# Optimization experiments

Measured on AMD Instinct MI355X. Metric: run time of the kernel, lower is better.

Reference implementation:

```python
import jax, jax.numpy as jnp
import numpy as np


def setup_inputs() -> dict:
    B, S, DK, DV, H = 2, 2048, 1024, 1024, 16
    ks = jax.random.split(jax.random.key(0), 7)
    keys = jax.random.normal(ks[0], (B, S, DK), jnp.float32)
    queries = jax.random.normal(ks[1], (B, S, DK), jnp.float32)
    values = jax.random.normal(ks[2], (B, S, DV), jnp.float32)
    # per-head projection weights, stored as [H, in, out] (torch Linear uses W.T; math-equivalent)
    WQ = jax.random.normal(ks[3], (H, DK, DK // H), jnp.float32) / np.sqrt(DK).astype(np.float32)
    WK = jax.random.normal(ks[4], (H, DK, DK // H), jnp.float32) / np.sqrt(DK).astype(np.float32)
    WV = jax.random.normal(ks[5], (H, DV, DV // H), jnp.float32) / np.sqrt(DV).astype(np.float32)
    WO = jax.random.normal(ks[6], (DV, DV), jnp.float32) / np.sqrt(DV).astype(np.float32)
    return {"keys": keys, "queries": queries, "values": values,
            "WQ": WQ, "WK": WK, "WV": WV, "WO": WO, "masking": 1}


def reference(keys, queries, values, WQ, WK, WV, WO, masking):
    B, Sq, _ = queries.shape
    Sk = keys.shape[1]
    # batched per-head projections (original loops over heads in Python)
    Q = jnp.einsum('bqd,hde->bhqe', queries, WQ)   # [B,H,Sq,dh]
    K = jnp.einsum('bkd,hde->bhke', keys, WK)      # [B,H,Sk,dh]
    V = jnp.einsum('bkd,hde->bhke', values, WV)    # [B,H,Sk,dvh]
    q_idx = jnp.arange(Sq)[:, None]
    k_idx = jnp.arange(Sk)[None, :]
    causal = k_idx <= q_idx
    # NOTE: original never applies the slope m; bias = (i - j) for i<=j else 0, same for all heads
    bias = jnp.where(causal, (k_idx - q_idx).astype(jnp.float32), 0.0)
    scale = np.float32(1.0 / np.sqrt(Sk))  # original divides by sqrt(keys.shape[1])
    y = (jnp.einsum('bhqe,bhke->bhqk', Q, K) + bias) * scale
    if masking:
        y = jnp.where(causal, y, -jnp.inf)
    # original: F.softmax(y, 1) on [B,Sq,Sk] -> softmax over the QUERY axis
    z = jax.nn.softmax(y, axis=2)
    out = jnp.einsum('bhqk,bhke->bhqe', z, V)      # [B,H,Sq,dvh]
    out = out.transpose(0, 2, 1, 3).reshape(B, Sq, -1)  # concat heads on last dim
    return out @ WO
```

## Files before the change

### kernel.cpp

```cpp
#include <hip/hip_runtime.h>
#include <math.h>

#define SEQ    2048
#define DMODEL 1024
#define NH     16
#define DH     64
#define NB     2
#define BHN    (NB*NH)

static constexpr float SCALE = 0.02209708691207961f;

typedef __attribute__((ext_vector_type(8))) short short8;
typedef __attribute__((ext_vector_type(4))) short short4v;
typedef __attribute__((ext_vector_type(4))) float f32x4;

__device__ __forceinline__ short f2bf(float f) {
    union { float f; unsigned u; } v; v.f = f;
    unsigned r = (v.u + 0x7FFFu + ((v.u >> 16) & 1u)) >> 16;
    return (short)r;
}

__device__ __forceinline__ unsigned pack_bf2(float a, float b) {
    union { float f; unsigned u; } ua, ub; ua.f = a; ub.f = b;
    return __builtin_amdgcn_perm(ub.u + 0x8000u, ua.u + 0x8000u, 0x07060302u);
}

__device__ __forceinline__ float bf2f(short s) {
    union { unsigned u; float f; } v; v.u = ((unsigned)(unsigned short)s) << 16;
    return v.f;
}

__device__ __forceinline__ void load16_lds(const short* g, short* l) {
    __builtin_amdgcn_global_load_lds(
        (const __attribute__((address_space(1))) unsigned int*)g,
        (__attribute__((address_space(3))) unsigned int*)l,
        16, 0, 0);
}

__device__ __forceinline__ void stage_rows(const short* g, short* s, int t, int ldg, int nIter) {
    int wave = t >> 6, lane = t & 63;
    #pragma unroll
    for (int i = 0; i < 4; ++i) {
        if (i >= nIter) break;
        int E   = i * 2048 + wave * 512 + lane * 8;
        int row = E >> 6;
        int blk = (lane & 7) ^ (row & 7);
        load16_lds(g + (size_t)row * ldg + blk * 8, s + i * 2048 + wave * 512);
    }
}

__device__ __forceinline__ short8 frag_sw(const short* s, int rowbase, int ks, int lane) {
    int m   = rowbase + (lane & 15);
    int q   = lane >> 4;
    int blk = (ks * 4 + q) ^ (m & 7);
    return *(const short8*)(s + m * 64 + blk * 8);
}

__device__ __forceinline__ void swizzle_tile(int x, int y, int& tile, int& bh) {
    int r = y >> 3;
    bh = (y & 7) * 4 + r;
    int xs = (r & 2) ? ((x + 16) & 31) : x;
    tile = (r & 1) ? (31 - xs) : xs;
}

__global__ __launch_bounds__(256) void convert_x(
    const float* __restrict__ q, const float* __restrict__ k, const float* __restrict__ v,
    short* __restrict__ Xq, short* __restrict__ Xk, short* __restrict__ Xv)
{
    const int z = blockIdx.z;
    const float* src = (z == 0) ? q : (z == 1) ? k : v;
    short* dst = (z == 0) ? Xq : (z == 1) ? Xk : Xv;
    size_t idx = ((size_t)blockIdx.x * 256 + threadIdx.x) * 8;
    float4 a = *(const float4*)(src + idx);
    float4 b = *(const float4*)(src + idx + 4);
    short8 o;
    o[0] = f2bf(a.x); o[1] = f2bf(a.y); o[2] = f2bf(a.z); o[3] = f2bf(a.w);
    o[4] = f2bf(b.x); o[5] = f2bf(b.y); o[6] = f2bf(b.z); o[7] = f2bf(b.w);
    *(short8*)(dst + idx) = o;
}

__global__ __launch_bounds__(256) void convert_w(
    const float* __restrict__ WQ, const float* __restrict__ WK,
    const float* __restrict__ WV, const float* __restrict__ WO,
    short* __restrict__ WQt, short* __restrict__ WKt,
    short* __restrict__ WVt, short* __restrict__ WOt)
{
    const int z = blockIdx.z;
    const int k0 = blockIdx.x * 64;
    const int ny = blockIdx.y;
    const float* W = (z == 0) ? WQ : (z == 1) ? WK : (z == 2) ? WV : WO;
    short* Wt = (z == 0) ? WQt : (z == 1) ? WKt : (z == 2) ? WVt : WOt;

    __shared__ float Ts[64][68];
    const int t = threadIdx.x;
    const int tr = t >> 4, tc4 = (t & 15) * 4;

    #pragma unroll
    for (int i = 0; i < 4; ++i) {
        int row = tr + i * 16;
        float4 v;
        if (z < 3) v = *(const float4*)(W + (size_t)ny * DMODEL * DH + (size_t)(k0 + row) * DH + tc4);
        else       v = *(const float4*)(W + (size_t)(k0 + row) * DMODEL + ny * 64 + tc4);
        Ts[tc4 + 0][row] = v.x; Ts[tc4 + 1][row] = v.y;
        Ts[tc4 + 2][row] = v.z; Ts[tc4 + 3][row] = v.w;
    }
    __syncthreads();
    #pragma unroll
    for (int i = 0; i < 4; ++i) {
        int nl = tr + i * 16;
        short4v o;
        o[0] = f2bf(Ts[nl][tc4 + 0]); o[1] = f2bf(Ts[nl][tc4 + 1]);
        o[2] = f2bf(Ts[nl][tc4 + 2]); o[3] = f2bf(Ts[nl][tc4 + 3]);
        *(short4v*)(Wt + (size_t)(ny * 64 + nl) * DMODEL + k0 + tc4) = o;
    }
}

__global__ __launch_bounds__(256) void gemm_nt(
    const short* __restrict__ A0, const short* __restrict__ A1, const short* __restrict__ A2,
    const short* __restrict__ B0, const short* __restrict__ B1, const short* __restrict__ B2,
    short* __restrict__ Y0, short* __restrict__ Y1, short* __restrict__ Y2,
    float* __restrict__ outF, int phase)
{
    const int z = blockIdx.z;
    const short* X  = (phase == 1) ? A0 : (z == 0) ? A0 : (z == 1) ? A1 : A2;
    const short* Wt = (phase == 1) ? B0 : (z == 0) ? B0 : (z == 1) ? B1 : B2;
    short* Y        = (z == 0) ? Y0 : (z == 1) ? Y1 : Y2;
    const bool vOrient = (phase == 0) && (z == 2);

    const int n0 = blockIdx.x * 128;
    const int m0 = blockIdx.y * 128;

    __shared__ short As[128 * 64];
    __shared__ short Bs[128 * 64];

    const int t = threadIdx.x;
    const int wave = t >> 6, lane = t & 63;
    const int wrow = (wave >> 1) * 64, wcol = (wave & 1) * 64;
    const int quad = lane >> 4, l15 = lane & 15;

    f32x4 acc[4][4];
    #pragma unroll
    for (int i = 0; i < 4; ++i)
        #pragma unroll
        for (int j = 0; j < 4; ++j)
            acc[i][j] = (f32x4)0.f;

    for (int k0 = 0; k0 < DMODEL; k0 += 64) {
        __syncthreads();
        stage_rows(X  + (size_t)m0 * DMODEL + k0, As, t, DMODEL, 4);
        stage_rows(Wt + (size_t)n0 * DMODEL + k0, Bs, t, DMODEL, 4);
        __syncthreads();
        if (!vOrient) {
            #pragma unroll
            for (int ks = 0; ks < 2; ++ks) {
                short8 xf[4], wf[4];
                #pragma unroll
                for (int i = 0; i < 4; ++i) xf[i] = frag_sw(As, wrow + i * 16, ks, lane);
                #pragma unroll
                for (int i = 0; i < 4; ++i) wf[i] = frag_sw(Bs, wcol + i * 16, ks, lane);
                #pragma unroll
                for (int a = 0; a < 4; ++a)
                    #pragma unroll
                    for (int b = 0; b < 4; ++b)
                        acc[a][b] = __builtin_amdgcn_mfma_f32_16x16x32_bf16(
                            wf[a], xf[b], acc[a][b], 0, 0, 0);
            }
        } else {
            #pragma unroll
            for (int ks = 0; ks < 2; ++ks) {
                short8 xf[4], wf[4];
                #pragma unroll
                for (int i = 0; i < 4; ++i) xf[i] = frag_sw(As, wrow + i * 16, ks, lane);
                #pragma unroll
                for (int i = 0; i < 4; ++i) wf[i] = frag_sw(Bs, wcol + i * 16, ks, lane);
                #pragma unroll
                for (int a = 0; a < 4; ++a)
                    #pragma unroll
                    for (int b = 0; b < 4; ++b)
                        acc[a][b] = __builtin_amdgcn_mfma_f32_16x16x32_bf16(
                            xf[a], wf[b], acc[a][b], 0, 0, 0);
            }
        }
    }

    if (vOrient) {
        #pragma unroll
        for (int a = 0; a < 4; ++a) {
            #pragma unroll
            for (int b = 0; b < 4; ++b) {
                int m = m0 + wrow + a * 16 + quad * 4;
                int n = n0 + wcol + b * 16 + l15;
                int bb = m >> 11, s = m & 2047, h = n >> 6, e = n & 63;
                short4v o;
                #pragma unroll
                for (int i = 0; i < 4; ++i) o[i] = f2bf(acc[a][b][i]);
                *(short4v*)(Y + ((size_t)((bb * NH + h) * DH + e)) * SEQ + s) = o;
            }
        }
    } else if (phase == 1) {
        #pragma unroll
        for (int a = 0; a < 4; ++a) {
            #pragma unroll
            for (int b = 0; b < 4; ++b) {
                int n = n0 + wcol + a * 16 + quad * 4;
                int m = m0 + wrow + b * 16 + l15;
                float4 o = make_float4(acc[a][b][0], acc[a][b][1], acc[a][b][2], acc[a][b][3]);
                *(float4*)(outF + (size_t)m * DMODEL + n) = o;
            }
        }
    } else {
        #pragma unroll
        for (int a = 0; a < 4; ++a) {
            #pragma unroll
            for (int b = 0; b < 4; ++b) {
                int n = n0 + wcol + a * 16 + quad * 4;
                int m = m0 + wrow + b * 16 + l15;
                int bb = m >> 11, s = m & 2047, h = n >> 6, e = n & 63;
                short4v o;
                #pragma unroll
                for (int i = 0; i < 4; ++i) o[i] = f2bf(acc[a][b][i]);
                *(short4v*)(Y + ((size_t)((bb * NH + h) * SEQ + s)) * DH + e) = o;
            }
        }
    }
}

__global__ __launch_bounds__(256) void stats_mfma(
    const short* __restrict__ Qg, const short* __restrict__ Kg,
    float* __restrict__ rDg, const int* __restrict__ mask_p)
{
    int kt, bh;
    swizzle_tile(blockIdx.x, blockIdx.y, kt, bh);
    const int k0 = kt * 64;
    const int masking = mask_p[0];

    __shared__ short Ks[64 * 64];
    __shared__ short Qs[2][128 * 64];

    const int t = threadIdx.x;
    const int wave = t >> 6, lane = t & 63;
    const int quad = lane >> 4, l15 = lane & 15;

    const int qb0 = masking ? (kt >> 1) : 0;
    const int q0s = qb0 * 128;
    stage_rows(Kg + ((size_t)bh * SEQ + k0) * DH, Ks, t, DH, 2);
    stage_rows(Qg + ((size_t)bh * SEQ + q0s) * DH, Qs[0], t, DH, 4);
    __syncthreads();

    short8 Kf[2];
    Kf[0] = frag_sw(Ks, wave * 16, 0, lane);
    Kf[1] = frag_sw(Ks, wave * 16, 1, lane);

    int   kgi[4];
    float biasK[4];
    #pragma unroll
    for (int i = 0; i < 4; ++i) {
        kgi[i] = k0 + wave * 16 + quad * 4 + i;
        biasK[i] = SCALE * (float)kgi[i];
    }
    float qS[8];
    #pragma unroll
    for (int nt = 0; nt < 8; ++nt)
        qS[nt] = SCALE * (float)(q0s + nt * 16 + l15);

    float dsum[4] = {0.f, 0.f, 0.f, 0.f};
    const int nIter = masking ? (16 - qb0) : 16;
    for (int it = 0; it < nIter; ++it) {
        const int cur = it & 1;
        if (it > 0) __syncthreads();
        if (it + 1 < nIter)
            stage_rows(Qg + ((size_t)bh * SEQ + q0s + (it + 1) * 128) * DH, Qs[1 - cur], t, DH, 4);

        f32x4 acc[8];
        #pragma unroll
        for (int nt = 0; nt < 8; ++nt) acc[nt] = (f32x4)0.f;
        __builtin_amdgcn_s_setprio(1);
        #pragma unroll
        for (int ks = 0; ks < 2; ++ks)
            #pragma unroll
            for (int nt = 0; nt < 8; ++nt)
                acc[nt] = __builtin_amdgcn_mfma_f32_16x16x32_bf16(
                    Kf[ks], frag_sw(Qs[cur], nt * 16, ks, lane), acc[nt], 0, 0, 0);
        __builtin_amdgcn_s_setprio(0);

        const bool exact = masking && (it == 0);
        #pragma unroll
        for (int nt = 0; nt < 8; ++nt) {
            #pragma unroll
            for (int i = 0; i < 4; ++i) {
                float diff = biasK[i] - qS[nt];
                float v = masking ? fmaf(acc[nt][i], SCALE, diff)
                                  : fmaf(acc[nt][i], SCALE, fminf(diff, 0.f));
                float e = __expf(v);
                if (exact)
                    e = (kgi[i] <= (q0s + nt * 16 + l15)) ? e : 0.f;
                dsum[i] += e;
            }
        }
        #pragma unroll
        for (int nt = 0; nt < 8; ++nt) qS[nt] += 128.f * SCALE;
    }

    #pragma unroll
    for (int i = 0; i < 4; ++i) {
        float d = dsum[i];
        #pragma unroll
        for (int mm = 1; mm < 16; mm <<= 1) d += __shfl_xor(d, mm);
        dsum[i] = d;
    }
    if (l15 == 0) {
        const int kc = k0 + wave * 16 + quad * 4;
        float4 o = make_float4(1.f / dsum[0], 1.f / dsum[1], 1.f / dsum[2], 1.f / dsum[3]);
        *(float4*)(rDg + (size_t)bh * SEQ + kc) = o;
    }
}

__global__ __launch_bounds__(256) void scale_vt(
    short* __restrict__ Vt, const float* __restrict__ rDg)
{
    size_t base = ((size_t)blockIdx.x * 256 + threadIdx.x) * 8;
    int s = (int)(base & (SEQ - 1));
    int bh = (int)(base >> 17);
    short8 v = *(short8*)(Vt + base);
    const float* rp = rDg + (size_t)bh * SEQ + s;
    float4 r0 = *(const float4*)rp;
    float4 r1 = *(const float4*)(rp + 4);
    float rr[8] = {r0.x, r0.y, r0.z, r0.w, r1.x, r1.y, r1.z, r1.w};
    union { unsigned u[4]; short8 s8; } o;
    #pragma unroll
    for (int j = 0; j < 4; ++j)
        o.u[j] = pack_bf2(bf2f(v[2 * j]) * rr[2 * j], bf2f(v[2 * j + 1]) * rr[2 * j + 1]);
    *(short8*)(Vt + base) = o.s8;
}

template<int MODE>
__device__ __forceinline__ void attn_tile(
    const short* Kbuf, const short* Vbuf, short* Pw,
    const short8 Qf[2], const float bias[4][4], f32x4 oacc[4],
    int lane, int quad, int l15, int qloc)
{
    f32x4 sacc[4];
    #pragma unroll
    for (int mt = 0; mt < 4; ++mt) sacc[mt] = (f32x4)0.f;
    #pragma unroll
    for (int ks = 0; ks < 2; ++ks) {
        #pragma unroll
        for (int mt = 0; mt < 4; ++mt)
            sacc[mt] = __builtin_amdgcn_mfma_f32_16x16x32_bf16(
                frag_sw(Kbuf, mt * 16, ks, lane), Qf[ks], sacc[mt], 0, 0, 0);
    }
    __asm__ volatile("" ::: "memory");
    #pragma unroll
    for (int mt = 0; mt < 4; ++mt) {
        float p[4];
        #pragma unroll
        for (int i = 0; i < 4; ++i) {
            float bi = bias[mt][i];
            float v = (MODE == 2) ? fmaf(sacc[mt][i], SCALE, fminf(bi, 0.f))
                                  : fmaf(sacc[mt][i], SCALE, bi);
            float e = __expf(v);
            if (MODE == 1)
                e = ((mt * 16 + quad * 4 + i) <= qloc) ? e : 0.f;
            p[i] = e;
        }
        int blk = (2 * mt + (quad >> 1)) ^ (l15 & 7);
        *(uint2*)(Pw + l15 * 64 + blk * 8 + (quad & 1) * 4) =
            make_uint2(pack_bf2(p[0], p[1]), pack_bf2(p[2], p[3]));
    }
    __asm__ volatile("" ::: "memory");
    #pragma unroll
    for (int ks = 0; ks < 2; ++ks) {
        short8 pf = *(const short8*)(Pw + l15 * 64 + (((ks * 4 + quad) ^ (l15 & 7)) * 8));
        #pragma unroll
        for (int mt = 0; mt < 4; ++mt)
            oacc[mt] = __builtin_amdgcn_mfma_f32_16x16x32_bf16(
                frag_sw(Vbuf, mt * 16, ks, lane), pf, oacc[mt], 0, 0, 0);
    }
}

__global__ __launch_bounds__(256) void attn_mfma(
    const short* __restrict__ Qg, const short* __restrict__ Kg, const short* __restrict__ Vt,
    short* __restrict__ attnb, const int* __restrict__ mask_p)
{
    int qt, bh;
    swizzle_tile(blockIdx.x, blockIdx.y, qt, bh);
    const int b = bh / NH, h = bh % NH;
    const int q0 = qt * 64;
    const int masking = mask_p[0];

    __shared__ short Qs[64 * 64];
    __shared__ short Ks[2][64 * 64];
    __shared__ short Vts[2][64 * 64];

    const int t = threadIdx.x;
    const int wave = t >> 6, lane = t & 63;
    const int quad = lane >> 4, l15 = lane & 15;
    short* Pw = Qs + wave * 1024;
    const int qloc = wave * 16 + l15;

    stage_rows(Qg + ((size_t)bh * SEQ + q0) * DH, Qs, t, DH, 2);
    stage_rows(Kg + (size_t)bh * SEQ * DH, Ks[0], t, DH, 2);
    stage_rows(Vt + (size_t)bh * DH * SEQ, Vts[0], t, SEQ, 2);
    __syncthreads();

    short8 Qf[2];
    Qf[0] = frag_sw(Qs, wave * 16, 0, lane);
    Qf[1] = frag_sw(Qs, wave * 16, 1, lane);

    float bias[4][4];
    #pragma unroll
    for (int mt = 0; mt < 4; ++mt)
        #pragma unroll
        for (int i = 0; i < 4; ++i)
            bias[mt][i] = SCALE * (float)((mt * 16 + quad * 4 + i)
                                        - (q0 + qloc));

    f32x4 oacc[4];
    #pragma unroll
    for (int mt = 0; mt < 4; ++mt) oacc[mt] = (f32x4)0.f;

    const int nIter = masking ? (qt + 1) : (SEQ / 64);
    for (int it = 0; it < nIter; ++it) {
        const int cur = it & 1;
        if (it > 0) __syncthreads();
        if (it + 1 < nIter) {
            const int k0n = (it + 1) * 64;
            stage_rows(Kg + ((size_t)bh * SEQ + k0n) * DH, Ks[1 - cur], t, DH, 2);
            stage_rows(Vt + (size_t)bh * DH * SEQ + k0n, Vts[1 - cur], t, SEQ, 2);
        }
        if (!masking)       attn_tile<2>(Ks[cur], Vts[cur], Pw, Qf, bias, oacc, lane, quad, l15, qloc);
        else if (it == qt)  attn_tile<1>(Ks[cur], Vts[cur], Pw, Qf, bias, oacc, lane, quad, l15, qloc);
        else                attn_tile<0>(Ks[cur], Vts[cur], Pw, Qf, bias, oacc, lane, quad, l15, qloc);
        #pragma unroll
        for (int mt = 0; mt < 4; ++mt)
            #pragma unroll
            for (int i = 0; i < 4; ++i)
                bias[mt][i] += 64.f * SCALE;
    }

    #pragma unroll
    for (int mt = 0; mt < 4; ++mt) {
        int e = mt * 16 + quad * 4;
        int q = q0 + wave * 16 + l15;
        short4v o;
        #pragma unroll
        for (int i = 0; i < 4; ++i) o[i] = f2bf(oacc[mt][i]);
        *(short4v*)(attnb + ((size_t)(b * SEQ + q)) * DMODEL + h * DH + e) = o;
    }
}

extern "C" void kernel_launch(void* const* d_in, const int* in_sizes, int n_in,
                              void* d_out, int out_size, void* d_ws, size_t ws_size,
                              hipStream_t stream) {
    const float* keys    = (const float*)d_in[0];
    const float* queries = (const float*)d_in[1];
    const float* values  = (const float*)d_in[2];
    const float* WQ      = (const float*)d_in[3];
    const float* WK      = (const float*)d_in[4];
    const float* WV      = (const float*)d_in[5];
    const float* WO      = (const float*)d_in[6];
    const int*   mask_p  = (const int*)d_in[7];
    float* out = (float*)d_out;

    const size_t nX = (size_t)NB * SEQ * DMODEL;
    const size_t nW = (size_t)DMODEL * DMODEL;
    const size_t nQ = (size_t)BHN * SEQ * DH;

    short* ws = (short*)d_ws;
    short* Xq    = ws;
    short* Xk    = Xq + nX;
    short* Xv    = Xk + nX;
    short* WQt   = Xv + nX;
    short* WKt   = WQt + nW;
    short* WVt   = WKt + nW;
    short* WOt   = WVt + nW;
    short* Qg    = WOt + nW;
    short* Kg    = Qg + nQ;
    short* Vtg   = Kg + nQ;
    short* attnb = Vtg + nQ;
    float* rDg   = (float*)(attnb + nX);

    convert_x<<<dim3(2048, 1, 3), dim3(256), 0, stream>>>(queries, keys, values, Xq, Xk, Xv);
    convert_w<<<dim3(16, 16, 4), dim3(256), 0, stream>>>(WQ, WK, WV, WO, WQt, WKt, WVt, WOt);
    gemm_nt<<<dim3(8, 32, 3), dim3(256), 0, stream>>>(
        Xq, Xk, Xv, WQt, WKt, WVt, Qg, Kg, Vtg, nullptr, 0);
    stats_mfma<<<dim3(32, 32), dim3(256), 0, stream>>>(Qg, Kg, rDg, mask_p);
    scale_vt<<<dim3(2048), dim3(256), 0, stream>>>(Vtg, rDg);
    attn_mfma<<<dim3(32, 32), dim3(256), 0, stream>>>(Qg, Kg, Vtg, attnb, mask_p);
    gemm_nt<<<dim3(8, 32, 1), dim3(256), 0, stream>>>(
        attnb, nullptr, nullptr, WOt, nullptr, nullptr, nullptr, nullptr, nullptr, out, 1);
}
```

Baseline: 270.1 us.

## Double query tile per attention block to reuse K/V fragments across two row groups

The attention kernel now processes 128 query rows per block, with each wave handling two 16-row groups, so every K and V fragment read from LDS feeds two MFMAs. This halves the number of blocks and the K/V staging traffic per query row. It also wraps the MFMA phases in s_setprio hints and adds per-wave causal tile skipping. In exchange it raises register pressure, halves the grid to 512 blocks (fewer waves resident to hide latency), and leaves idle waves on diagonal tiles where some waves skip their work.

```diff
diff --git a/kernel.cpp b/kernel.cpp
--- a/kernel.cpp
+++ b/kernel.cpp
@@ -61,6 +61,13 @@
     bh = (y & 7) * 4 + r;
     int xs = (r & 2) ? ((x + 16) & 31) : x;
     tile = (r & 1) ? (31 - xs) : xs;
+}
+
+__device__ __forceinline__ void swizzle_tile16(int x, int y, int& tile, int& bh) {
+    int r = y >> 3;
+    bh = (y & 7) * 4 + r;
+    int xs = (r & 1) ? ((x + 8) & 15) : x;
+    tile = (r & 2) ? (15 - xs) : xs;
 }
 
 __global__ __launch_bounds__(256) void convert_x(
@@ -334,48 +341,71 @@
 }
 
 template<int MODE>
-__device__ __forceinline__ void attn_tile(
+__device__ __forceinline__ void attn_tile2(
     const short* Kbuf, const short* Vbuf, short* Pw,
-    const short8 Qf[2], const float bias[4][4], f32x4 oacc[4],
-    int lane, int quad, int l15, int qloc)
-{
-    f32x4 sacc[4];
-    #pragma unroll
-    for (int mt = 0; mt < 4; ++mt) sacc[mt] = (f32x4)0.f;
+    const short8 Qf[2][2], const float biasK[4][4], const float qS[2],
+    const int qgi[2], int kbase, f32x4 oacc[4][2],
+    int lane, int quad, int l15)
+{
+    f32x4 sacc[4][2];
+    #pragma unroll
+    for (int mt = 0; mt < 4; ++mt)
+        #pragma unroll
+        for (int g = 0; g < 2; ++g) sacc[mt][g] = (f32x4)0.f;
+    __builtin_amdgcn_s_setprio(1);
     #pragma unroll
     for (int ks = 0; ks < 2; ++ks) {
         #pragma unroll
-        for (int mt = 0; mt < 4; ++mt)
-            sacc[mt] = __builtin_amdgcn_mfma_f32_16x16x32_bf16(
-                frag_sw(Kbuf, mt * 16, ks, lane), Qf[ks], sacc[mt], 0, 0, 0);
-    }
+        for (int mt = 0; mt < 4; ++mt) {
+            short8 kf = frag_sw(Kbuf, mt * 16, ks, lane);
+            #pragma unroll
+            for (int g = 0; g < 2; ++g)
+                sacc[mt][g] = __builtin_amdgcn_mfma_f32_16x16x32_bf16(
+                    kf, Qf[g][ks], sacc[mt][g], 0, 0, 0);
+        }
+    }
+    __builtin_amdgcn_s_setprio(0);
     __asm__ volatile("" ::: "memory");
     #pragma unroll
     for (int mt = 0; mt < 4; ++mt) {
-        float p[4];
-        #pragma unroll
-        for (int i = 0; i < 4; ++i) {
-            float bi = bias[mt][i];
-            float v = (MODE == 2) ? fmaf(sacc[mt][i], SCALE, fminf(bi, 0.f))
-                                  : fmaf(sacc[mt][i], SCALE, bi);
-            float e = __expf(v);
-            if (MODE == 1)
-                e = ((mt * 16 + quad * 4 + i) <= qloc) ? e : 0.f;
-            p[i] = e;
-        }
-        int blk = (2 * mt + (quad >> 1)) ^ (l15 & 7);
-        *(uint2*)(Pw + l15 * 64 + blk * 8 + (quad & 1) * 4) =
-            make_uint2(pack_bf2(p[0], p[1]), pack_bf2(p[2], p[3]));
+        #pragma unroll
+        for (int g = 0; g < 2; ++g) {
+            float p[4];
+            #pragma unroll
+            for (int i = 0; i < 4; ++i) {
+                float diff = biasK[mt][i] - qS[g];
+                float v = (MODE == 2) ? fmaf(sacc[mt][g][i], SCALE, fminf(diff, 0.f))
+                                      : fmaf(sacc[mt][g][i], SCALE, diff);
+                float e = __expf(v);
+                if (MODE == 1)
+                    e = ((kbase + mt * 16 + quad * 4 + i) <= qgi[g]) ? e : 0.f;
+                p[i] = e;
+            }
+            int row = g * 16 + l15;
+            int blk = (2 * mt + (quad >> 1)) ^ (l15 & 7);
+            *(uint2*)(Pw + row * 64 + blk * 8 + (quad & 1) * 4) =
+                make_uint2(pack_bf2(p[0], p[1]), pack_bf2(p[2], p[3]));
+        }
     }
     __asm__ volatile("" ::: "memory");
+    __builtin_amdgcn_s_setprio(1);
     #pragma unroll
     for (int ks = 0; ks < 2; ++ks) {
-        short8 pf = *(const short8*)(Pw + l15 * 64 + (((ks * 4 + quad) ^ (l15 & 7)) * 8));
-        #pragma unroll
-        for (int mt = 0; mt < 4; ++mt)
-            oacc[mt] = __builtin_amdgcn_mfma_f32_16x16x32_bf16(
-                frag_sw(Vbuf, mt * 16, ks, lane), pf, oacc[mt], 0, 0, 0);
-    }
+        short8 pf[2];
+        #pragma unroll
+        for (int g = 0; g < 2; ++g)
+            pf[g] = *(const short8*)(Pw + (g * 16 + l15) * 64
+                                     + (((ks * 4 + quad) ^ (l15 & 7)) * 8));
+        #pragma unroll
+        for (int mt = 0; mt < 4; ++mt) {
+            short8 vf = frag_sw(Vbuf, mt * 16, ks, lane);
+            #pragma unroll
+            for (int g = 0; g < 2; ++g)
+                oacc[mt][g] = __builtin_amdgcn_mfma_f32_16x16x32_bf16(
+                    vf, pf[g], oacc[mt][g], 0, 0, 0);
+        }
+    }
+    __builtin_amdgcn_s_setprio(0);
 }
 
 __global__ __launch_bounds__(256) void attn_mfma(
@@ -383,43 +413,53 @@
     short* __restrict__ attnb, const int* __restrict__ mask_p)
 {
     int qt, bh;
-    swizzle_tile(blockIdx.x, blockIdx.y, qt, bh);
+    swizzle_tile16(blockIdx.x, blockIdx.y, qt, bh);
     const int b = bh / NH, h = bh % NH;
-    const int q0 = qt * 64;
+    const int q0 = qt * 128;
     const int masking = mask_p[0];
 
-    __shared__ short Qs[64 * 64];
+    __shared__ short Qs[128 * 64];
     __shared__ short Ks[2][64 * 64];
     __shared__ short Vts[2][64 * 64];
 
     const int t = threadIdx.x;
     const int wave = t >> 6, lane = t & 63;
     const int quad = lane >> 4, l15 = lane & 15;
-    short* Pw = Qs + wave * 1024;
-    const int qloc = wave * 16 + l15;
-
-    stage_rows(Qg + ((size_t)bh * SEQ + q0) * DH, Qs, t, DH, 2);
+    short* Pw = Qs + wave * 2048;
+
+    stage_rows(Qg + ((size_t)bh * SEQ + q0) * DH, Qs, t, DH, 4);
     stage_rows(Kg + (size_t)bh * SEQ * DH, Ks[0], t, DH, 2);
     stage_rows(Vt + (size_t)bh * DH * SEQ, Vts[0], t, SEQ, 2);
     __syncthreads();
 
-    short8 Qf[2];
-    Qf[0] = frag_sw(Qs, wave * 16, 0, lane);
-    Qf[1] = frag_sw(Qs, wave * 16, 1, lane);
-
-    float bias[4][4];
+    short8 Qf[2][2];
+    #pragma unroll
+    for (int g = 0; g < 2; ++g) {
+        Qf[g][0] = frag_sw(Qs, wave * 32 + g * 16, 0, lane);
+        Qf[g][1] = frag_sw(Qs, wave * 32 + g * 16, 1, lane);
+    }
+
+    int   qgi[2];
+    float qS[2];
+    #pragma unroll
+    for (int g = 0; g < 2; ++g) {
+        qgi[g] = q0 + wave * 32 + g * 16 + l15;
+        qS[g]  = SCALE * (float)qgi[g];
+    }
+    float biasK[4][4];
     #pragma unroll
     for (int mt = 0; mt < 4; ++mt)
         #pragma unroll
         for (int i = 0; i < 4; ++i)
-            bias[mt][i] = SCALE * (float)((mt * 16 + quad * 4 + i)
-                                        - (q0 + qloc));
-
-    f32x4 oacc[4];
-    #pragma unroll
-    for (int mt = 0; mt < 4; ++mt) oacc[mt] = (f32x4)0.f;
-
-    const int nIter = masking ? (qt + 1) : (SEQ / 64);
+            biasK[mt][i] = SCALE * (float)(mt * 16 + quad * 4 + i);
+
+    f32x4 oacc[4][2];
+    #pragma unroll
+    for (int mt = 0; mt < 4; ++mt)
+        #pragma unroll
+        for (int g = 0; g < 2; ++g) oacc[mt][g] = (f32x4)0.f;
+
+    const int nIter = masking ? (2 * qt + 2) : (SEQ / 64);
     for (int it = 0; it < nIter; ++it) {
         const int cur = it & 1;
         if (it > 0) __syncthreads();
@@ -428,24 +468,34 @@
             stage_rows(Kg + ((size_t)bh * SEQ + k0n) * DH, Ks[1 - cur], t, DH, 2);
             stage_rows(Vt + (size_t)bh * DH * SEQ + k0n, Vts[1 - cur], t, SEQ, 2);
         }
-        if (!masking)       attn_tile<2>(Ks[cur], Vts[cur], Pw, Qf, bias, oacc, lane, quad, l15, qloc);
-        else if (it == qt)  attn_tile<1>(Ks[cur], Vts[cur], Pw, Qf, bias, oacc, lane, quad, l15, qloc);
-        else                attn_tile<0>(Ks[cur], Vts[cur], Pw, Qf, bias, oacc, lane, quad, l15, qloc);
+        if (!masking) {
+            attn_tile2<2>(Ks[cur], Vts[cur], Pw, Qf, biasK, qS, qgi, 64 * it,
+                          oacc, lane, quad, l15);
+        } else if (64 * it + 63 <= q0 + 32 * wave) {
+            attn_tile2<0>(Ks[cur], Vts[cur], Pw, Qf, biasK, qS, qgi, 64 * it,
+                          oacc, lane, quad, l15);
+        } else if (64 * it <= q0 + 32 * wave + 31) {
+            attn_tile2<1>(Ks[cur], Vts[cur], Pw, Qf, biasK, qS, qgi, 64 * it,
+                          oacc, lane, quad, l15);
+        }
         #pragma unroll
         for (int mt = 0; mt < 4; ++mt)
             #pragma unroll
             for (int i = 0; i < 4; ++i)
-                bias[mt][i] += 64.f * SCALE;
+                biasK[mt][i] += 64.f * SCALE;
     }
 
     #pragma unroll
     for (int mt = 0; mt < 4; ++mt) {
-        int e = mt * 16 + quad * 4;
-        int q = q0 + wave * 16 + l15;
-        short4v o;
-        #pragma unroll
-        for (int i = 0; i < 4; ++i) o[i] = f2bf(oacc[mt][i]);
-        *(short4v*)(attnb + ((size_t)(b * SEQ + q)) * DMODEL + h * DH + e) = o;
+        #pragma unroll
+        for (int g = 0; g < 2; ++g) {
+            int e = mt * 16 + quad * 4;
+            int q = q0 + wave * 32 + g * 16 + l15;
+            short4v o;
+            #pragma unroll
+            for (int i = 0; i < 4; ++i) o[i] = f2bf(oacc[mt][g][i]);
+            *(short4v*)(attnb + ((size_t)(b * SEQ + q)) * DMODEL + h * DH + e) = o;
+        }
     }
 }
 
@@ -486,7 +536,7 @@
         Xq, Xk, Xv, WQt, WKt, WVt, Qg, Kg, Vtg, nullptr, 0);
     stats_mfma<<<dim3(32, 32), dim3(256), 0, stream>>>(Qg, Kg, rDg, mask_p);
     scale_vt<<<dim3(2048), dim3(256), 0, stream>>>(Vtg, rDg);
-    attn_mfma<<<dim3(32, 32), dim3(256), 0, stream>>>(Qg, Kg, Vtg, attnb, mask_p);
+    attn_mfma<<<dim3(16, 32), dim3(256), 0, stream>>>(Qg, Kg, Vtg, attnb, mask_p);
     gemm_nt<<<dim3(8, 32, 1), dim3(256), 0, stream>>>(
         attnb, nullptr, nullptr, WOt, nullptr, nullptr, nullptr, nullptr, nullptr, out, 1);
 }
```

Result: no change. 269.7 us (-0.2%).

## Load attention K/V fragments directly from global memory, drop LDS staging

Applied to the files above, without the earlier changes.

The attention kernel no longer stages Q, K and V^T tiles into double-buffered shared memory with barriers. Each wave now loads its MFMA fragments straight from global memory (relying on L1/L2 for reuse across the four waves), and only the per-wave P scratch stays in LDS. It also raises wave priority around the MFMA blocks with s_setprio. This removes __syncthreads and LDS traffic and raises occupancy, at the cost of redundant global/L2 loads per wave, less coalesced strided V^T accesses, and no software prefetch to hide latency.

```diff
diff --git a/kernel.cpp b/kernel.cpp
--- a/kernel.cpp
+++ b/kernel.cpp
@@ -54,6 +54,12 @@
     int q   = lane >> 4;
     int blk = (ks * 4 + q) ^ (m & 7);
     return *(const short8*)(s + m * 64 + blk * 8);
+}
+
+__device__ __forceinline__ short8 frag_g(const short* base, int stride, int rowbase, int ks, int lane) {
+    int m = rowbase + (lane & 15);
+    int c = (lane >> 4) * 8 + ks * 32;
+    return *(const short8*)(base + (size_t)m * stride + c);
 }
 
 __device__ __forceinline__ void swizzle_tile(int x, int y, int& tile, int& bh) {
@@ -334,21 +340,23 @@
 }
 
 template<int MODE>
-__device__ __forceinline__ void attn_tile(
-    const short* Kbuf, const short* Vbuf, short* Pw,
+__device__ __forceinline__ void attn_tile_g(
+    const short* Kp, const short* Vp, short* Pw,
     const short8 Qf[2], const float bias[4][4], f32x4 oacc[4],
     int lane, int quad, int l15, int qloc)
 {
     f32x4 sacc[4];
     #pragma unroll
     for (int mt = 0; mt < 4; ++mt) sacc[mt] = (f32x4)0.f;
+    __builtin_amdgcn_s_setprio(1);
     #pragma unroll
     for (int ks = 0; ks < 2; ++ks) {
         #pragma unroll
         for (int mt = 0; mt < 4; ++mt)
             sacc[mt] = __builtin_amdgcn_mfma_f32_16x16x32_bf16(
-                frag_sw(Kbuf, mt * 16, ks, lane), Qf[ks], sacc[mt], 0, 0, 0);
-    }
+                frag_g(Kp, DH, mt * 16, ks, lane), Qf[ks], sacc[mt], 0, 0, 0);
+    }
+    __builtin_amdgcn_s_setprio(0);
     __asm__ volatile("" ::: "memory");
     #pragma unroll
     for (int mt = 0; mt < 4; ++mt) {
@@ -368,14 +376,16 @@
             make_uint2(pack_bf2(p[0], p[1]), pack_bf2(p[2], p[3]));
     }
     __asm__ volatile("" ::: "memory");
+    __builtin_amdgcn_s_setprio(1);
     #pragma unroll
     for (int ks = 0; ks < 2; ++ks) {
         short8 pf = *(const short8*)(Pw + l15 * 64 + (((ks * 4 + quad) ^ (l15 & 7)) * 8));
         #pragma unroll
         for (int mt = 0; mt < 4; ++mt)
             oacc[mt] = __builtin_amdgcn_mfma_f32_16x16x32_bf16(
-                frag_sw(Vbuf, mt * 16, ks, lane), pf, oacc[mt], 0, 0, 0);
-    }
+                frag_g(Vp, SEQ, mt * 16, ks, lane), pf, oacc[mt], 0, 0, 0);
+    }
+    __builtin_amdgcn_s_setprio(0);
 }
 
 __global__ __launch_bounds__(256) void attn_mfma(
@@ -388,24 +398,18 @@
     const int q0 = qt * 64;
     const int masking = mask_p[0];
 
-    __shared__ short Qs[64 * 64];
-    __shared__ short Ks[2][64 * 64];
-    __shared__ short Vts[2][64 * 64];
+    __shared__ short Ps[4 * 1024];
 
     const int t = threadIdx.x;
     const int wave = t >> 6, lane = t & 63;
     const int quad = lane >> 4, l15 = lane & 15;
-    short* Pw = Qs + wave * 1024;
+    short* Pw = Ps + wave * 1024;
     const int qloc = wave * 16 + l15;
 
-    stage_rows(Qg + ((size_t)bh * SEQ + q0) * DH, Qs, t, DH, 2);
-    stage_rows(Kg + (size_t)bh * SEQ * DH, Ks[0], t, DH, 2);
-    stage_rows(Vt + (size_t)bh * DH * SEQ, Vts[0], t, SEQ, 2);
-    __syncthreads();
-
+    const short* Qp = Qg + ((size_t)bh * SEQ + q0 + wave * 16) * DH;
     short8 Qf[2];
-    Qf[0] = frag_sw(Qs, wave * 16, 0, lane);
-    Qf[1] = frag_sw(Qs, wave * 16, 1, lane);
+    Qf[0] = frag_g(Qp, DH, 0, 0, lane);
+    Qf[1] = frag_g(Qp, DH, 0, 1, lane);
 
     float bias[4][4];
     #pragma unroll
@@ -419,18 +423,16 @@
     #pragma unroll
     for (int mt = 0; mt < 4; ++mt) oacc[mt] = (f32x4)0.f;
 
+    const short* Kp = Kg + (size_t)bh * SEQ * DH;
+    const short* Vp = Vt + (size_t)bh * DH * SEQ;
+
     const int nIter = masking ? (qt + 1) : (SEQ / 64);
     for (int it = 0; it < nIter; ++it) {
-        const int cur = it & 1;
-        if (it > 0) __syncthreads();
-        if (it + 1 < nIter) {
-            const int k0n = (it + 1) * 64;
-            stage_rows(Kg + ((size_t)bh * SEQ + k0n) * DH, Ks[1 - cur], t, DH, 2);
-            stage_rows(Vt + (size_t)bh * DH * SEQ + k0n, Vts[1 - cur], t, SEQ, 2);
-        }
-        if (!masking)       attn_tile<2>(Ks[cur], Vts[cur], Pw, Qf, bias, oacc, lane, quad, l15, qloc);
-        else if (it == qt)  attn_tile<1>(Ks[cur], Vts[cur], Pw, Qf, bias, oacc, lane, quad, l15, qloc);
-        else                attn_tile<0>(Ks[cur], Vts[cur], Pw, Qf, bias, oacc, lane, quad, l15, qloc);
+        const short* Kt = Kp + (size_t)it * 64 * DH;
+        const short* Vc = Vp + it * 64;
+        if (!masking)       attn_tile_g<2>(Kt, Vc, Pw, Qf, bias, oacc, lane, quad, l15, qloc);
+        else if (it == qt)  attn_tile_g<1>(Kt, Vc, Pw, Qf, bias, oacc, lane, quad, l15, qloc);
+        else                attn_tile_g<0>(Kt, Vc, Pw, Qf, bias, oacc, lane, quad, l15, qloc);
         #pragma unroll
         for (int mt = 0; mt < 4; ++mt)
             #pragma unroll
```

Result: slower. 347.3 us (+28.6%).

## Pair heavy and light causal tiles per block in stats and attention kernels

Applied to the files above, without the earlier changes.

Both stats_mfma and attn_mfma now launch 512 blocks. Each block processes two work items, w and 1023-w, so under the causal mask every block gets a roughly equal amount of work, replacing the earlier swizzled 32x32 grid. The attention tile also raises wave priority around its MFMA sections. This is meant to remove tail imbalance from triangular work. In exchange it halves the number of blocks, which may reduce occupancy and latency hiding on a GPU with 256 CUs.

```diff
diff --git a/kernel.cpp b/kernel.cpp
--- a/kernel.cpp
+++ b/kernel.cpp
@@ -54,13 +54,6 @@
     int q   = lane >> 4;
     int blk = (ks * 4 + q) ^ (m & 7);
     return *(const short8*)(s + m * 64 + blk * 8);
-}
-
-__device__ __forceinline__ void swizzle_tile(int x, int y, int& tile, int& bh) {
-    int r = y >> 3;
-    bh = (y & 7) * 4 + r;
-    int xs = (r & 2) ? ((x + 16) & 31) : x;
-    tile = (r & 1) ? (31 - xs) : xs;
 }
 
 __global__ __launch_bounds__(256) void convert_x(
@@ -229,9 +222,7 @@
     const short* __restrict__ Qg, const short* __restrict__ Kg,
     float* __restrict__ rDg, const int* __restrict__ mask_p)
 {
-    int kt, bh;
-    swizzle_tile(blockIdx.x, blockIdx.y, kt, bh);
-    const int k0 = kt * 64;
+    const int gblk = blockIdx.x;
     const int masking = mask_p[0];
 
     __shared__ short Ks[64 * 64];
@@ -241,77 +232,84 @@
     const int wave = t >> 6, lane = t & 63;
     const int quad = lane >> 4, l15 = lane & 15;
 
-    const int qb0 = masking ? (kt >> 1) : 0;
-    const int q0s = qb0 * 128;
-    stage_rows(Kg + ((size_t)bh * SEQ + k0) * DH, Ks, t, DH, 2);
-    stage_rows(Qg + ((size_t)bh * SEQ + q0s) * DH, Qs[0], t, DH, 4);
-    __syncthreads();
-
-    short8 Kf[2];
-    Kf[0] = frag_sw(Ks, wave * 16, 0, lane);
-    Kf[1] = frag_sw(Ks, wave * 16, 1, lane);
-
-    int   kgi[4];
-    float biasK[4];
-    #pragma unroll
-    for (int i = 0; i < 4; ++i) {
-        kgi[i] = k0 + wave * 16 + quad * 4 + i;
-        biasK[i] = SCALE * (float)kgi[i];
-    }
-    float qS[8];
-    #pragma unroll
-    for (int nt = 0; nt < 8; ++nt)
-        qS[nt] = SCALE * (float)(q0s + nt * 16 + l15);
-
-    float dsum[4] = {0.f, 0.f, 0.f, 0.f};
-    const int nIter = masking ? (16 - qb0) : 16;
-    for (int it = 0; it < nIter; ++it) {
-        const int cur = it & 1;
-        if (it > 0) __syncthreads();
-        if (it + 1 < nIter)
-            stage_rows(Qg + ((size_t)bh * SEQ + q0s + (it + 1) * 128) * DH, Qs[1 - cur], t, DH, 4);
-
-        f32x4 acc[8];
-        #pragma unroll
-        for (int nt = 0; nt < 8; ++nt) acc[nt] = (f32x4)0.f;
-        __builtin_amdgcn_s_setprio(1);
-        #pragma unroll
-        for (int ks = 0; ks < 2; ++ks)
-            #pragma unroll
-            for (int nt = 0; nt < 8; ++nt)
-                acc[nt] = __builtin_amdgcn_mfma_f32_16x16x32_bf16(
-                    Kf[ks], frag_sw(Qs[cur], nt * 16, ks, lane), acc[nt], 0, 0, 0);
-        __builtin_amdgcn_s_setprio(0);
-
-        const bool exact = masking && (it == 0);
-        #pragma unroll
-        for (int nt = 0; nt < 8; ++nt) {
-            #pragma unroll
-            for (int i = 0; i < 4; ++i) {
-                float diff = biasK[i] - qS[nt];
-                float v = masking ? fmaf(acc[nt][i], SCALE, diff)
-                                  : fmaf(acc[nt][i], SCALE, fminf(diff, 0.f));
-                float e = __expf(v);
-                if (exact)
-                    e = (kgi[i] <= (q0s + nt * 16 + l15)) ? e : 0.f;
-                dsum[i] += e;
-            }
-        }
-        #pragma unroll
-        for (int nt = 0; nt < 8; ++nt) qS[nt] += 128.f * SCALE;
-    }
-
-    #pragma unroll
-    for (int i = 0; i < 4; ++i) {
-        float d = dsum[i];
-        #pragma unroll
-        for (int mm = 1; mm < 16; mm <<= 1) d += __shfl_xor(d, mm);
-        dsum[i] = d;
-    }
-    if (l15 == 0) {
-        const int kc = k0 + wave * 16 + quad * 4;
-        float4 o = make_float4(1.f / dsum[0], 1.f / dsum[1], 1.f / dsum[2], 1.f / dsum[3]);
-        *(float4*)(rDg + (size_t)bh * SEQ + kc) = o;
+    for (int item = 0; item < 2; ++item) {
+        const int w  = item ? (1023 - gblk) : gblk;
+        const int kt = w >> 5, bh = w & 31;
+        const int k0 = kt * 64;
+
+        const int qb0 = masking ? (kt >> 1) : 0;
+        const int q0s = qb0 * 128;
+        if (item) __syncthreads();
+        stage_rows(Kg + ((size_t)bh * SEQ + k0) * DH, Ks, t, DH, 2);
+        stage_rows(Qg + ((size_t)bh * SEQ + q0s) * DH, Qs[0], t, DH, 4);
+        __syncthreads();
+
+        short8 Kf[2];
+        Kf[0] = frag_sw(Ks, wave * 16, 0, lane);
+        Kf[1] = frag_sw(Ks, wave * 16, 1, lane);
+
+        int   kgi[4];
+        float biasK[4];
+        #pragma unroll
+        for (int i = 0; i < 4; ++i) {
+            kgi[i] = k0 + wave * 16 + quad * 4 + i;
+            biasK[i] = SCALE * (float)kgi[i];
+        }
+        float qS[8];
+        #pragma unroll
+        for (int nt = 0; nt < 8; ++nt)
+            qS[nt] = SCALE * (float)(q0s + nt * 16 + l15);
+
+        float dsum[4] = {0.f, 0.f, 0.f, 0.f};
+        const int nIter = masking ? (16 - qb0) : 16;
+        for (int it = 0; it < nIter; ++it) {
+            const int cur = it & 1;
+            if (it > 0) __syncthreads();
+            if (it + 1 < nIter)
+                stage_rows(Qg + ((size_t)bh * SEQ + q0s + (it + 1) * 128) * DH, Qs[1 - cur], t, DH, 4);
+
+            f32x4 acc[8];
+            #pragma unroll
+            for (int nt = 0; nt < 8; ++nt) acc[nt] = (f32x4)0.f;
+            __builtin_amdgcn_s_setprio(1);
+            #pragma unroll
+            for (int ks = 0; ks < 2; ++ks)
+                #pragma unroll
+                for (int nt = 0; nt < 8; ++nt)
+                    acc[nt] = __builtin_amdgcn_mfma_f32_16x16x32_bf16(
+                        Kf[ks], frag_sw(Qs[cur], nt * 16, ks, lane), acc[nt], 0, 0, 0);
+            __builtin_amdgcn_s_setprio(0);
+
+            const bool exact = masking && (it == 0);
+            #pragma unroll
+            for (int nt = 0; nt < 8; ++nt) {
+                #pragma unroll
+                for (int i = 0; i < 4; ++i) {
+                    float diff = biasK[i] - qS[nt];
+                    float v = masking ? fmaf(acc[nt][i], SCALE, diff)
+                                      : fmaf(acc[nt][i], SCALE, fminf(diff, 0.f));
+                    float e = __expf(v);
+                    if (exact)
+                        e = (kgi[i] <= (q0s + nt * 16 + l15)) ? e : 0.f;
+                    dsum[i] += e;
+                }
+            }
+            #pragma unroll
+            for (int nt = 0; nt < 8; ++nt) qS[nt] += 128.f * SCALE;
+        }
+
+        #pragma unroll
+        for (int i = 0; i < 4; ++i) {
+            float d = dsum[i];
+            #pragma unroll
+            for (int mm = 1; mm < 16; mm <<= 1) d += __shfl_xor(d, mm);
+            dsum[i] = d;
+        }
+        if (l15 == 0) {
+            const int kc = k0 + wave * 16 + quad * 4;
+            float4 o = make_float4(1.f / dsum[0], 1.f / dsum[1], 1.f / dsum[2], 1.f / dsum[3]);
+            *(float4*)(rDg + (size_t)bh * SEQ + kc) = o;
+        }
     }
 }
 
@@ -342,6 +340,7 @@
     f32x4 sacc[4];
     #pragma unroll
     for (int mt = 0; mt < 4; ++mt) sacc[mt] = (f32x4)0.f;
+    __builtin_amdgcn_s_setprio(1);
     #pragma unroll
     for (int ks = 0; ks < 2; ++ks) {
         #pragma unroll
@@ -349,6 +348,7 @@
             sacc[mt] = __builtin_amdgcn_mfma_f32_16x16x32_bf16(
                 frag_sw(Kbuf, mt * 16, ks, lane), Qf[ks], sacc[mt], 0, 0, 0);
     }
+    __builtin_amdgcn_s_setprio(0);
     __asm__ volatile("" ::: "memory");
     #pragma unroll
     for (int mt = 0; mt < 4; ++mt) {
@@ -368,6 +368,7 @@
             make_uint2(pack_bf2(p[0], p[1]), pack_bf2(p[2], p[3]));
     }
     __asm__ volatile("" ::: "memory");
+    __builtin_amdgcn_s_setprio(1);
     #pragma unroll
     for (int ks = 0; ks < 2; ++ks) {
         short8 pf = *(const short8*)(Pw + l15 * 64 + (((ks * 4 + quad) ^ (l15 & 7)) * 8));
@@ -376,16 +377,14 @@
             oacc[mt] = __builtin_amdgcn_mfma_f32_16x16x32_bf16(
                 frag_sw(Vbuf, mt * 16, ks, lane), pf, oacc[mt], 0, 0, 0);
     }
+    __builtin_amdgcn_s_setprio(0);
 }
 
 __global__ __launch_bounds__(256) void attn_mfma(
     const short* __restrict__ Qg, const short* __restrict__ Kg, const short* __restrict__ Vt,
     short* __restrict__ attnb, const int* __restrict__ mask_p)
 {
-    int qt, bh;
-    swizzle_tile(blockIdx.x, blockIdx.y, qt, bh);
-    const int b = bh / NH, h = bh % NH;
-    const int q0 = qt * 64;
+    const int gblk = blockIdx.x;
     const int masking = mask_p[0];
 
     __shared__ short Qs[64 * 64];
@@ -398,54 +397,62 @@
     short* Pw = Qs + wave * 1024;
     const int qloc = wave * 16 + l15;
 
-    stage_rows(Qg + ((size_t)bh * SEQ + q0) * DH, Qs, t, DH, 2);
-    stage_rows(Kg + (size_t)bh * SEQ * DH, Ks[0], t, DH, 2);
-    stage_rows(Vt + (size_t)bh * DH * SEQ, Vts[0], t, SEQ, 2);
-    __syncthreads();
-
-    short8 Qf[2];
-    Qf[0] = frag_sw(Qs, wave * 16, 0, lane);
-    Qf[1] = frag_sw(Qs, wave * 16, 1, lane);
-
-    float bias[4][4];
-    #pragma unroll
-    for (int mt = 0; mt < 4; ++mt)
-        #pragma unroll
-        for (int i = 0; i < 4; ++i)
-            bias[mt][i] = SCALE * (float)((mt * 16 + quad * 4 + i)
-                                        - (q0 + qloc));
-
-    f32x4 oacc[4];
-    #pragma unroll
-    for (int mt = 0; mt < 4; ++mt) oacc[mt] = (f32x4)0.f;
-
-    const int nIter = masking ? (qt + 1) : (SEQ / 64);
-    for (int it = 0; it < nIter; ++it) {
-        const int cur = it & 1;
-        if (it > 0) __syncthreads();
-        if (it + 1 < nIter) {
-            const int k0n = (it + 1) * 64;
-            stage_rows(Kg + ((size_t)bh * SEQ + k0n) * DH, Ks[1 - cur], t, DH, 2);
-            stage_rows(Vt + (size_t)bh * DH * SEQ + k0n, Vts[1 - cur], t, SEQ, 2);
-        }
-        if (!masking)       attn_tile<2>(Ks[cur], Vts[cur], Pw, Qf, bias, oacc, lane, quad, l15, qloc);
-        else if (it == qt)  attn_tile<1>(Ks[cur], Vts[cur], Pw, Qf, bias, oacc, lane, quad, l15, qloc);
-        else                attn_tile<0>(Ks[cur], Vts[cur], Pw, Qf, bias, oacc, lane, quad, l15, qloc);
+    for (int item = 0; item < 2; ++item) {
+        const int w  = item ? (1023 - gblk) : gblk;
+        const int qt = w >> 5, bh = w & 31;
+        const int b = bh >> 4, h = bh & (NH - 1);
+        const int q0 = qt * 64;
+
+        if (item) __syncthreads();
+        stage_rows(Qg + ((size_t)bh * SEQ + q0) * DH, Qs, t, DH, 2);
+        stage_rows(Kg + (size_t)bh * SEQ * DH, Ks[0], t, DH, 2);
+        stage_rows(Vt + (size_t)bh * DH * SEQ, Vts[0], t, SEQ, 2);
+        __syncthreads();
+
+        short8 Qf[2];
+        Qf[0] = frag_sw(Qs, wave * 16, 0, lane);
+        Qf[1] = frag_sw(Qs, wave * 16, 1, lane);
+
+        float bias[4][4];
         #pragma unroll
         for (int mt = 0; mt < 4; ++mt)
             #pragma unroll
             for (int i = 0; i < 4; ++i)
-                bias[mt][i] += 64.f * SCALE;
-    }
-
-    #pragma unroll
-    for (int mt = 0; mt < 4; ++mt) {
-        int e = mt * 16 + quad * 4;
-        int q = q0 + wave * 16 + l15;
-        short4v o;
-        #pragma unroll
-        for (int i = 0; i < 4; ++i) o[i] = f2bf(oacc[mt][i]);
-        *(short4v*)(attnb + ((size_t)(b * SEQ + q)) * DMODEL + h * DH + e) = o;
+                bias[mt][i] = SCALE * (float)((mt * 16 + quad * 4 + i)
+                                            - (q0 + qloc));
+
+        f32x4 oacc[4];
+        #pragma unroll
+        for (int mt = 0; mt < 4; ++mt) oacc[mt] = (f32x4)0.f;
+
+        const int nIter = masking ? (qt + 1) : (SEQ / 64);
+        for (int it = 0; it < nIter; ++it) {
+            const int cur = it & 1;
+            if (it > 0) __syncthreads();
+            if (it + 1 < nIter) {
+                const int k0n = (it + 1) * 64;
+                stage_rows(Kg + ((size_t)bh * SEQ + k0n) * DH, Ks[1 - cur], t, DH, 2);
+                stage_rows(Vt + (size_t)bh * DH * SEQ + k0n, Vts[1 - cur], t, SEQ, 2);
+            }
+            if (!masking)       attn_tile<2>(Ks[cur], Vts[cur], Pw, Qf, bias, oacc, lane, quad, l15, qloc);
+            else if (it == qt)  attn_tile<1>(Ks[cur], Vts[cur], Pw, Qf, bias, oacc, lane, quad, l15, qloc);
+            else                attn_tile<0>(Ks[cur], Vts[cur], Pw, Qf, bias, oacc, lane, quad, l15, qloc);
+            #pragma unroll
+            for (int mt = 0; mt < 4; ++mt)
+                #pragma unroll
+                for (int i = 0; i < 4; ++i)
+                    bias[mt][i] += 64.f * SCALE;
+        }
+
+        #pragma unroll
+        for (int mt = 0; mt < 4; ++mt) {
+            int e = mt * 16 + quad * 4;
+            int q = q0 + wave * 16 + l15;
+            short4v o;
+            #pragma unroll
+            for (int i = 0; i < 4; ++i) o[i] = f2bf(oacc[mt][i]);
+            *(short4v*)(attnb + ((size_t)(b * SEQ + q)) * DMODEL + h * DH + e) = o;
+        }
     }
 }
 
@@ -484,9 +491,9 @@
     convert_w<<<dim3(16, 16, 4), dim3(256), 0, stream>>>(WQ, WK, WV, WO, WQt, WKt, WVt, WOt);
     gemm_nt<<<dim3(8, 32, 3), dim3(256), 0, stream>>>(
         Xq, Xk, Xv, WQt, WKt, WVt, Qg, Kg, Vtg, nullptr, 0);
-    stats_mfma<<<dim3(32, 32), dim3(256), 0, stream>>>(Qg, Kg, rDg, mask_p);
+    stats_mfma<<<dim3(512), dim3(256), 0, stream>>>(Qg, Kg, rDg, mask_p);
     scale_vt<<<dim3(2048), dim3(256), 0, stream>>>(Vtg, rDg);
-    attn_mfma<<<dim3(32, 32), dim3(256), 0, stream>>>(Qg, Kg, Vtg, attnb, mask_p);
+    attn_mfma<<<dim3(512), dim3(256), 0, stream>>>(Qg, Kg, Vtg, attnb, mask_p);
     gemm_nt<<<dim3(8, 32, 1), dim3(256), 0, stream>>>(
         attnb, nullptr, nullptr, WOt, nullptr, nullptr, nullptr, nullptr, nullptr, out, 1);
 }
```

Measured after the change: 262.5 us. 1.03x faster.
